# Kernel optimization log

Measured on AMD Instinct MI355X. Metric: run time of the kernel, lower is better.

The kernel has to match this reference:

```python
import jax, jax.numpy as jnp
import numpy as np


def _seg_mean(h_src, src, dst, n_dst):
    # gather neighbor features along edges, then segment-mean onto dst nodes
    msgs = h_src[src]                                  # [E, F]
    s = jax.ops.segment_sum(msgs, dst, num_segments=n_dst)
    deg = jax.ops.segment_sum(jnp.ones_like(dst, dtype=h_src.dtype), dst, num_segments=n_dst)
    return s / jnp.maximum(deg, 1.0)[:, None]          # zero-degree -> 0


def _sage_conv(h_src, h_dst, src, dst, n_dst, W, b):
    h_N = _seg_mean(h_src, src, dst, n_dst)            # [n_dst, F]
    h_total = jnp.concatenate([h_dst, h_N], axis=1)    # [n_dst, 2F]
    return h_total @ W + b


def setup_inputs() -> dict:
    key = jax.random.key(0)
    ks = jax.random.split(key, 10)
    n_src1, n_dst1, n_dst2 = 200000, 50000, 10000
    E1, E2 = 1000000, 200000
    in_f, h_f, n_cls = 256, 256, 64
    x = jax.random.normal(ks[0], (n_src1, in_f), dtype=jnp.float32)
    W1 = jax.random.normal(ks[1], (2 * in_f, h_f), dtype=jnp.float32) * (1.0 / np.sqrt(2 * in_f))
    b1 = jax.random.normal(ks[2], (h_f,), dtype=jnp.float32) * 0.01
    W2 = jax.random.normal(ks[3], (2 * h_f, n_cls), dtype=jnp.float32) * (1.0 / np.sqrt(2 * h_f))
    b2 = jax.random.normal(ks[4], (n_cls,), dtype=jnp.float32) * 0.01
    src1 = jax.random.randint(ks[5], (E1,), 0, n_src1, dtype=jnp.int32)
    dst1 = jax.random.randint(ks[6], (E1,), 0, n_dst1, dtype=jnp.int32)
    src2 = jax.random.randint(ks[7], (E2,), 0, n_dst1, dtype=jnp.int32)
    dst2 = jax.random.randint(ks[8], (E2,), 0, n_dst2, dtype=jnp.int32)
    return {"x": x, "W1": W1, "b1": b1, "W2": W2, "b2": b2,
            "src1": src1, "dst1": dst1, "src2": src2, "dst2": dst2,
            "n_dst1": n_dst1, "n_dst2": n_dst2}


def reference(x, W1, b1, W2, b2, src1, dst1, src2, dst2, n_dst1, n_dst2):
    h_dst = x[:n_dst1]
    h = _sage_conv(x, h_dst, src1, dst1, n_dst1, W1, b1)
    h = jax.nn.relu(h)
    h_dst2 = h[:n_dst2]
    out = _sage_conv(h, h_dst2, src2, dst2, n_dst2, W2, b2)
    return out
```

## Files before the change

### kernel.cpp

```cpp
#include <hip/hip_runtime.h>
#include <hip/hip_bf16.h>

#define N_DST1 50000
#define N_DST2 10000
#define FEAT   256

typedef unsigned int u32;
typedef __attribute__((ext_vector_type(4))) float f32x4;
typedef __attribute__((ext_vector_type(8))) short bf16x8;

__device__ __forceinline__ ushort f2bf(float f) {
    u32 u = __float_as_uint(f);
    u32 r = (u + 0x7FFFu + ((u >> 16) & 1u)) >> 16;
    return (ushort)r;
}
__device__ __forceinline__ float bf2f(ushort u) {
    return __uint_as_float(((u32)u) << 16);
}

__device__ __forceinline__ void gload_lds16(const void* g, void* l) {
    __builtin_amdgcn_global_load_lds(
        (const __attribute__((address_space(1))) u32*)g,
        (__attribute__((address_space(3))) u32*)l, 16, 0, 0);
}

__global__ __launch_bounds__(256) void prep_kernel(
    const float* __restrict__ x, ushort* __restrict__ xb, u32* __restrict__ xq,
    int n8, int n8h,
    const int* __restrict__ dst1, int E1, int* __restrict__ deg1,
    const int* __restrict__ dst2, int E2, int* __restrict__ deg2)
{
    int gid = blockIdx.x * blockDim.x + threadIdx.x;
    if (gid < n8) {
        const f32x4* p = (const f32x4*)x + (size_t)gid * 2;
        f32x4 a = __builtin_nontemporal_load(p);
        f32x4 b = __builtin_nontemporal_load(p + 1);
        if (xq) {
            u32 w0 = 0, w1 = 0;
            w0 = __builtin_amdgcn_cvt_pk_fp8_f32(a.x, a.y, w0, false);
            w0 = __builtin_amdgcn_cvt_pk_fp8_f32(a.z, a.w, w0, true);
            w1 = __builtin_amdgcn_cvt_pk_fp8_f32(b.x, b.y, w1, false);
            w1 = __builtin_amdgcn_cvt_pk_fp8_f32(b.z, b.w, w1, true);
            uint2 wv; wv.x = w0; wv.y = w1;
            *((uint2*)xq + gid) = wv;
        }
        if (gid < n8h) {
            ushort4 lo = make_ushort4(f2bf(a.x), f2bf(a.y), f2bf(a.z), f2bf(a.w));
            ushort4 hi = make_ushort4(f2bf(b.x), f2bf(b.y), f2bf(b.z), f2bf(b.w));
            ushort4* q = (ushort4*)xb + (size_t)gid * 2;
            q[0] = lo; q[1] = hi;
        }
    } else {
        int e = gid - n8;
        if (e < E1) atomicAdd(&deg1[dst1[e]], 1);
        else {
            int k = e - E1;
            if (k < E2) atomicAdd(&deg2[dst2[k]], 1);
        }
    }
}

__global__ __launch_bounds__(1024) void scan_wt_kernel(
    const int* __restrict__ degA, int nA, int* __restrict__ offA, int* __restrict__ posA,
    const int* __restrict__ degB, int nB, int* __restrict__ offB, int* __restrict__ posB,
    const float* __restrict__ W1, ushort* __restrict__ W1T,
    const float* __restrict__ W2, ushort* __restrict__ W2T)
{
    if (blockIdx.x >= 2) {
        int k = blockIdx.x - 2;
        int t = threadIdx.x;
        if (t < 256) W1T[(size_t)t * 512 + k] = f2bf(W1[(size_t)k * 256 + t]);
        else if (t < 320) {
            int n = t - 256;
            W2T[(size_t)n * 512 + k] = f2bf(W2[(size_t)k * 64 + n]);
        }
        return;
    }
    const int* deg = (blockIdx.x == 0) ? degA : degB;
    int*       off = (blockIdx.x == 0) ? offA : offB;
    int*       pos = (blockIdx.x == 0) ? posA : posB;
    int n = (blockIdx.x == 0) ? nA : nB;
    int n4 = n >> 2;

    __shared__ int wsum[16];
    __shared__ int carry_s;
    int t = threadIdx.x;
    int lane = t & 63, wid = t >> 6;
    if (t == 0) carry_s = 0;
    __syncthreads();
    for (int base = 0; base < n4; base += 1024) {
        int i = base + t;
        int4 v = make_int4(0, 0, 0, 0);
        if (i < n4) v = reinterpret_cast<const int4*>(deg)[i];
        int tot = v.x + v.y + v.z + v.w;
        int s = tot;
        #pragma unroll
        for (int d = 1; d < 64; d <<= 1) {
            int u = __shfl_up(s, d, 64);
            if (lane >= d) s += u;
        }
        if (lane == 63) wsum[wid] = s;
        __syncthreads();
        if (wid == 0 && lane < 16) {
            int ws = wsum[lane];
            #pragma unroll
            for (int d = 1; d < 16; d <<= 1) {
                int u = __shfl_up(ws, d, 64);
                if (lane >= d) ws += u;
            }
            wsum[lane] = ws;
        }
        __syncthreads();
        int waveoff = (wid == 0) ? 0 : wsum[wid - 1];
        int carry = carry_s;
        int base0 = carry + waveoff + s - tot;
        if (i < n4) {
            int4 e;
            e.x = base0;
            e.y = base0 + v.x;
            e.z = base0 + v.x + v.y;
            e.w = base0 + v.x + v.y + v.z;
            reinterpret_cast<int4*>(off)[i] = e;
            reinterpret_cast<int4*>(pos)[i] = e;
        }
        __syncthreads();
        if (t == 0) carry_s = carry + wsum[15];
        __syncthreads();
    }
    if (t == 0) off[n] = carry_s;
}

__global__ void scatter_csr2_kernel(const int* __restrict__ src1, const int* __restrict__ dst1,
                                    int E1, int* __restrict__ pos1, int* __restrict__ csr1,
                                    const int* __restrict__ src2, const int* __restrict__ dst2,
                                    int E2, int* __restrict__ pos2, int* __restrict__ csr2) {
    int i = blockIdx.x * blockDim.x + threadIdx.x;
    if (i < E1) {
        int slot = atomicAdd(&pos1[dst1[i]], 1);
        csr1[slot] = src1[i];
    } else {
        int k = i - E1;
        if (k < E2) {
            int slot = atomicAdd(&pos2[dst2[k]], 1);
            csr2[slot] = src2[k];
        }
    }
}

__global__ __launch_bounds__(512) void seg_mean_fp8_kernel(
    const u32* __restrict__ Xq, const int* __restrict__ off,
    const int* __restrict__ csr, ushort* __restrict__ out, int ndst)
{
    int wid = threadIdx.x >> 6;
    int d = blockIdx.x * 8 + wid;
    if (d >= ndst) return;
    int l = threadIdx.x & 63;
    int sub = l >> 4;
    int lg = l & 15;
    int beg = off[d], end = off[d + 1];
    float acc[16];
    #pragma unroll
    for (int q = 0; q < 16; ++q) acc[q] = 0.f;
    for (int j = beg; j < end; j += 4) {
        int idx = j + sub;
        int r = csr[min(idx, end - 1)];
        uint4 v = *reinterpret_cast<const uint4*>(Xq + (size_t)r * 64 + lg * 4);
        float m = (idx < end) ? 1.f : 0.f;
        u32 wv[4] = {v.x, v.y, v.z, v.w};
        #pragma unroll
        for (int w = 0; w < 4; ++w) {
            auto p01 = __builtin_amdgcn_cvt_pk_f32_fp8(wv[w], false);
            auto p23 = __builtin_amdgcn_cvt_pk_f32_fp8(wv[w], true);
            acc[w * 4 + 0] += m * p01[0];
            acc[w * 4 + 1] += m * p01[1];
            acc[w * 4 + 2] += m * p23[0];
            acc[w * 4 + 3] += m * p23[1];
        }
    }
    #pragma unroll
    for (int q = 0; q < 16; ++q) {
        acc[q] += __shfl_xor(acc[q], 16);
        acc[q] += __shfl_xor(acc[q], 32);
    }
    if (l < 16) {
        float sc = 1.0f / (float)max(end - beg, 1);
        bf16x8 o0, o1;
        #pragma unroll
        for (int q = 0; q < 8; ++q) {
            o0[q] = (short)f2bf(acc[q] * sc);
            o1[q] = (short)f2bf(acc[8 + q] * sc);
        }
        ushort* base = out + (size_t)d * FEAT + lg * 16;
        *reinterpret_cast<bf16x8*>(base) = o0;
        *reinterpret_cast<bf16x8*>(base + 8) = o1;
    }
}

__global__ __launch_bounds__(512) void seg_mean_bf16_kernel(
    const ushort* __restrict__ X, const int* __restrict__ off,
    const int* __restrict__ csr, ushort* __restrict__ out, int ndst)
{
    int wid = threadIdx.x >> 6;
    int d = blockIdx.x * 8 + wid;
    if (d >= ndst) return;
    int l = threadIdx.x & 63;
    int half = l >> 5;
    int f8 = (l & 31) * 8;
    int beg = off[d], end = off[d + 1];
    float acc[8] = {0.f, 0.f, 0.f, 0.f, 0.f, 0.f, 0.f, 0.f};
    for (int j = beg; j < end; j += 8) {
        #pragma unroll
        for (int p = 0; p < 4; ++p) {
            int idx = j + p * 2 + half;
            int r = csr[min(idx, end - 1)];
            bf16x8 v = *reinterpret_cast<const bf16x8*>(&X[(size_t)r * FEAT + f8]);
            float m = (idx < end) ? 1.f : 0.f;
            #pragma unroll
            for (int q = 0; q < 8; ++q) acc[q] += m * bf2f((ushort)v[q]);
        }
    }
    #pragma unroll
    for (int q = 0; q < 8; ++q) acc[q] += __shfl_xor(acc[q], 32);
    if (l < 32) {
        float sc = 1.0f / (float)max(end - beg, 1);
        bf16x8 ov;
        #pragma unroll
        for (int q = 0; q < 8; ++q) ov[q] = (short)f2bf(acc[q] * sc);
        *reinterpret_cast<bf16x8*>(&out[(size_t)d * FEAT + f8]) = ov;
    }
}

__global__ void seg_mean_f32_kernel(const float* __restrict__ X, const int* __restrict__ off,
                                    const int* __restrict__ csr, ushort* __restrict__ out) {
    int d = blockIdx.x;
    int t = threadIdx.x;
    int beg = off[d], end = off[d + 1];
    float a0 = 0.f, a1 = 0.f, a2 = 0.f, a3 = 0.f;
    for (int j = beg; j < end; ++j) {
        int s = csr[j];
        float4 v = *reinterpret_cast<const float4*>(&X[(size_t)s * FEAT + t * 4]);
        a0 += v.x; a1 += v.y; a2 += v.z; a3 += v.w;
    }
    float sc = 1.0f / (float)max(end - beg, 1);
    ushort4 o = make_ushort4(f2bf(a0 * sc), f2bf(a1 * sc), f2bf(a2 * sc), f2bf(a3 * sc));
    *reinterpret_cast<ushort4*>(&out[(size_t)d * FEAT + t * 4]) = o;
}

template<int BM, int BN, int WGM, int WGN, bool RELU, bool OBF16>
__global__ __launch_bounds__(WGM * WGN * 64)
void gemm_mfma_kernel(const ushort* __restrict__ A0, const ushort* __restrict__ A1,
                      const ushort* __restrict__ BT, const float* __restrict__ bias,
                      ushort* __restrict__ Cb, float* __restrict__ Cf,
                      int M, int Nfull) {
    constexpr int NWAVE = WGM * WGN;
    constexpr int WM = BM / WGM;
    constexpr int WN = BN / WGN;
    constexpr int MF = WM / 16;
    constexpr int NF = WN / 16;
    constexpr int ACH = BM / 16;
    constexpr int BCH = BN / 16;

    __shared__ ushort Al[2][BM][32];
    __shared__ ushort Bl[2][BN][32];

    const int t = threadIdx.x;
    const int lane = t & 63;
    const int wid = t >> 6;
    const int wm = wid / WGN, wn = wid % WGN;
    const int lr = lane & 15, grp = lane >> 4;
    const int rowBase = blockIdx.y * BM;
    const int colBase = blockIdx.x * BN;

    f32x4 acc[MF][NF];
    #pragma unroll
    for (int m = 0; m < MF; ++m)
        #pragma unroll
        for (int n = 0; n < NF; ++n)
            acc[m][n] = (f32x4){0.f, 0.f, 0.f, 0.f};

    auto stage = [&](int buf, int kt) {
        const ushort* Asrc = (kt < 8) ? A0 : A1;
        const int kcol = (kt * 32) & 255;
        #pragma unroll
        for (int ch = wid; ch < ACH; ch += NWAVE) {
            int r = ch * 16 + (lane >> 2);
            int rg = min(rowBase + r, M - 1);
            int c = lane & 3;
            int ksw = (c ^ (r & 3)) * 8;
            gload_lds16(&Asrc[(size_t)rg * 256 + kcol + ksw], &Al[buf][ch * 16][0]);
        }
        #pragma unroll
        for (int ch = wid; ch < BCH; ch += NWAVE) {
            int r = ch * 16 + (lane >> 2);
            int c = lane & 3;
            int ksw = (c ^ (r & 3)) * 8;
            gload_lds16(&BT[(size_t)(colBase + r) * 512 + kt * 32 + ksw], &Bl[buf][ch * 16][0]);
        }
    };

    stage(0, 0);
    __syncthreads();

    int buf = 0;
    for (int kt = 0; kt < 16; ++kt) {
        if (kt + 1 < 16) stage(buf ^ 1, kt + 1);
        bf16x8 af[MF], bfr[NF];
        #pragma unroll
        for (int m = 0; m < MF; ++m) {
            int r = wm * WM + m * 16 + lr;
            af[m] = *reinterpret_cast<const bf16x8*>(
                (const char*)&Al[buf][0][0] + r * 64 + ((grp ^ (r & 3)) << 4));
        }
        #pragma unroll
        for (int n = 0; n < NF; ++n) {
            int r = wn * WN + n * 16 + lr;
            bfr[n] = *reinterpret_cast<const bf16x8*>(
                (const char*)&Bl[buf][0][0] + r * 64 + ((grp ^ (r & 3)) << 4));
        }
        #pragma unroll
        for (int m = 0; m < MF; ++m)
            #pragma unroll
            for (int n = 0; n < NF; ++n)
                acc[m][n] = __builtin_amdgcn_mfma_f32_16x16x32_bf16(af[m], bfr[n], acc[m][n], 0, 0, 0);
        __syncthreads();
        buf ^= 1;
    }

    #pragma unroll
    for (int m = 0; m < MF; ++m) {
        #pragma unroll
        for (int q = 0; q < 4; ++q) {
            int rowg = rowBase + wm * WM + m * 16 + grp * 4 + q;
            if (rowg >= M) continue;
            #pragma unroll
            for (int n = 0; n < NF; ++n) {
                int colg = colBase + wn * WN + n * 16 + lr;
                float v = acc[m][n][q] + bias[colg];
                if (RELU) v = fmaxf(v, 0.f);
                if (OBF16) Cb[(size_t)rowg * Nfull + colg] = f2bf(v);
                else       Cf[(size_t)rowg * Nfull + colg] = v;
            }
        }
    }
}

extern "C" void kernel_launch(void* const* d_in, const int* in_sizes, int n_in,
                              void* d_out, int out_size, void* d_ws, size_t ws_size,
                              hipStream_t stream) {
    const float* x  = (const float*)d_in[0];
    const float* W1 = (const float*)d_in[1];
    const float* b1 = (const float*)d_in[2];
    const float* W2 = (const float*)d_in[3];
    const float* b2 = (const float*)d_in[4];
    const int* src1 = (const int*)d_in[5];
    const int* dst1 = (const int*)d_in[6];
    const int* src2 = (const int*)d_in[7];
    const int* dst2 = (const int*)d_in[8];
    const int E1 = in_sizes[5];
    const int E2 = in_sizes[7];
    const int N_SRC1 = in_sizes[0] / FEAT;
    float* out = (float*)d_out;

    char* ws = (char*)d_ws;
    size_t o = 0;
    auto carve = [&](size_t bytes) { char* p = ws + o; o = (o + bytes + 255) & ~(size_t)255; return p; };
    int*    degs = (int*)   carve((size_t)(N_DST1 + N_DST2) * 4);
    int*    deg1 = degs;
    int*    deg2 = degs + N_DST1;
    int*    off1 = (int*)   carve((size_t)(N_DST1 + 1) * 4);
    int*    pos1 = (int*)   carve((size_t)N_DST1 * 4);
    int*    csr1 = (int*)   carve((size_t)E1 * 4);
    ushort* hN1b = (ushort*)carve((size_t)N_DST1 * FEAT * 2);
    ushort* hb   = (ushort*)carve((size_t)N_DST1 * FEAT * 2);
    int*    off2 = (int*)   carve((size_t)(N_DST2 + 1) * 4);
    int*    pos2 = (int*)   carve((size_t)N_DST2 * 4);
    int*    csr2 = (int*)   carve((size_t)E2 * 4);
    ushort* hN2b = (ushort*)carve((size_t)N_DST2 * FEAT * 2);
    ushort* W1T  = (ushort*)carve((size_t)256 * 512 * 2);
    ushort* W2T  = (ushort*)carve((size_t)64 * 512 * 2);
    ushort* xb = (ushort*)carve((size_t)N_DST1 * FEAT * 2);
    size_t q_bytes = (size_t)N_SRC1 * FEAT;
    bool fp8path = (o + q_bytes) <= ws_size;
    u32* xq = fp8path ? (u32*)carve(q_bytes) : nullptr;

    (void)hipMemsetAsync(degs, 0, (size_t)(N_DST1 + N_DST2) * 4, stream);
    {
        int n8  = (fp8path ? N_SRC1 : N_DST1) * FEAT / 8;
        int n8h = N_DST1 * FEAT / 8;
        int tot = n8 + E1 + E2;
        prep_kernel<<<(tot + 255) / 256, 256, 0, stream>>>(
            x, xb, xq, n8, n8h, dst1, E1, deg1, dst2, E2, deg2);
    }
    scan_wt_kernel<<<514, 1024, 0, stream>>>(deg1, N_DST1, off1, pos1,
                                             deg2, N_DST2, off2, pos2,
                                             W1, W1T, W2, W2T);
    scatter_csr2_kernel<<<(E1 + E2 + 255) / 256, 256, 0, stream>>>(
        src1, dst1, E1, pos1, csr1, src2, dst2, E2, pos2, csr2);

    if (fp8path)
        seg_mean_fp8_kernel<<<(N_DST1 + 7) / 8, 512, 0, stream>>>(xq, off1, csr1, hN1b, N_DST1);
    else
        seg_mean_f32_kernel<<<N_DST1, 64, 0, stream>>>(x, off1, csr1, hN1b);
    gemm_mfma_kernel<128, 128, 2, 2, true, true><<<dim3(2, (N_DST1 + 127) / 128), 256, 0, stream>>>(
        xb, hN1b, W1T, b1, hb, nullptr, N_DST1, 256);

    seg_mean_bf16_kernel<<<(N_DST2 + 7) / 8, 512, 0, stream>>>(hb, off2, csr2, hN2b, N_DST2);
    gemm_mfma_kernel<64, 64, 2, 2, false, false><<<dim3(1, (N_DST2 + 63) / 64), 256, 0, stream>>>(
        hb, hN2b, W2T, b2, nullptr, out, N_DST2, 64);
}
```

Baseline: 310.7 us.

## Vectorize edge loops by four, unroll fp8 gather by two, widen GEMM1 tile

The degree-count and CSR scatter kernels now have each thread load int4 vectors of dst/src and issue four atomics, so fewer threads launch and index loads are wider. The fp8 segment-mean loop handles two neighbor rows per sub-lane per iteration to keep more gathers in flight. The first GEMM moves to a 128x256 tile with 512 threads, so one block covers the whole output width and A is loaded once. The wider GEMM tile lowers the block count to about 391 and may raise register pressure. The unrolled gather uses more registers.

```diff
diff --git a/kernel.cpp b/kernel.cpp
--- a/kernel.cpp
+++ b/kernel.cpp
@@ -50,14 +50,29 @@
             ushort4* q = (ushort4*)xb + (size_t)gid * 2;
             q[0] = lo; q[1] = hi;
         }
-    } else {
-        int e = gid - n8;
-        if (e < E1) atomicAdd(&deg1[dst1[e]], 1);
-        else {
-            int k = e - E1;
-            if (k < E2) atomicAdd(&deg2[dst2[k]], 1);
-        }
-    }
+        return;
+    }
+    int e = gid - n8;
+    int e14 = E1 >> 2, e24 = E2 >> 2;
+    if (e < e14) {
+        int4 d4 = reinterpret_cast<const int4*>(dst1)[e];
+        atomicAdd(&deg1[d4.x], 1); atomicAdd(&deg1[d4.y], 1);
+        atomicAdd(&deg1[d4.z], 1); atomicAdd(&deg1[d4.w], 1);
+        return;
+    }
+    e -= e14;
+    if (e < e24) {
+        int4 d4 = reinterpret_cast<const int4*>(dst2)[e];
+        atomicAdd(&deg2[d4.x], 1); atomicAdd(&deg2[d4.y], 1);
+        atomicAdd(&deg2[d4.z], 1); atomicAdd(&deg2[d4.w], 1);
+        return;
+    }
+    e -= e24;
+    int r1 = E1 & 3;
+    if (e < r1) { atomicAdd(&deg1[dst1[E1 - r1 + e]], 1); return; }
+    e -= r1;
+    int r2 = E2 & 3;
+    if (e < r2) { atomicAdd(&deg2[dst2[E2 - r2 + e]], 1); return; }
 }
 
 __global__ __launch_bounds__(1024) void scan_wt_kernel(
@@ -134,16 +149,40 @@
                                     int E1, int* __restrict__ pos1, int* __restrict__ csr1,
                                     const int* __restrict__ src2, const int* __restrict__ dst2,
                                     int E2, int* __restrict__ pos2, int* __restrict__ csr2) {
-    int i = blockIdx.x * blockDim.x + threadIdx.x;
-    if (i < E1) {
-        int slot = atomicAdd(&pos1[dst1[i]], 1);
-        csr1[slot] = src1[i];
-    } else {
-        int k = i - E1;
-        if (k < E2) {
-            int slot = atomicAdd(&pos2[dst2[k]], 1);
-            csr2[slot] = src2[k];
-        }
+    int e = blockIdx.x * blockDim.x + threadIdx.x;
+    int e14 = E1 >> 2, e24 = E2 >> 2;
+    if (e < e14) {
+        int4 s4 = reinterpret_cast<const int4*>(src1)[e];
+        int4 d4 = reinterpret_cast<const int4*>(dst1)[e];
+        csr1[atomicAdd(&pos1[d4.x], 1)] = s4.x;
+        csr1[atomicAdd(&pos1[d4.y], 1)] = s4.y;
+        csr1[atomicAdd(&pos1[d4.z], 1)] = s4.z;
+        csr1[atomicAdd(&pos1[d4.w], 1)] = s4.w;
+        return;
+    }
+    e -= e14;
+    if (e < e24) {
+        int4 s4 = reinterpret_cast<const int4*>(src2)[e];
+        int4 d4 = reinterpret_cast<const int4*>(dst2)[e];
+        csr2[atomicAdd(&pos2[d4.x], 1)] = s4.x;
+        csr2[atomicAdd(&pos2[d4.y], 1)] = s4.y;
+        csr2[atomicAdd(&pos2[d4.z], 1)] = s4.z;
+        csr2[atomicAdd(&pos2[d4.w], 1)] = s4.w;
+        return;
+    }
+    e -= e24;
+    int r1 = E1 & 3;
+    if (e < r1) {
+        int i = E1 - r1 + e;
+        csr1[atomicAdd(&pos1[dst1[i]], 1)] = src1[i];
+        return;
+    }
+    e -= r1;
+    int r2 = E2 & 3;
+    if (e < r2) {
+        int i = E2 - r2 + e;
+        csr2[atomicAdd(&pos2[dst2[i]], 1)] = src2[i];
+        return;
     }
 }
 
@@ -161,20 +200,26 @@
     float acc[16];
     #pragma unroll
     for (int q = 0; q < 16; ++q) acc[q] = 0.f;
-    for (int j = beg; j < end; j += 4) {
-        int idx = j + sub;
-        int r = csr[min(idx, end - 1)];
-        uint4 v = *reinterpret_cast<const uint4*>(Xq + (size_t)r * 64 + lg * 4);
-        float m = (idx < end) ? 1.f : 0.f;
-        u32 wv[4] = {v.x, v.y, v.z, v.w};
+    for (int j = beg; j < end; j += 8) {
+        int i0 = j + sub, i1 = j + 4 + sub;
+        int r0 = csr[min(i0, end - 1)];
+        int r1 = csr[min(i1, end - 1)];
+        uint4 v0 = *reinterpret_cast<const uint4*>(Xq + (size_t)r0 * 64 + lg * 4);
+        uint4 v1 = *reinterpret_cast<const uint4*>(Xq + (size_t)r1 * 64 + lg * 4);
+        float m0 = (i0 < end) ? 1.f : 0.f;
+        float m1 = (i1 < end) ? 1.f : 0.f;
+        u32 w0[4] = {v0.x, v0.y, v0.z, v0.w};
+        u32 w1[4] = {v1.x, v1.y, v1.z, v1.w};
         #pragma unroll
         for (int w = 0; w < 4; ++w) {
-            auto p01 = __builtin_amdgcn_cvt_pk_f32_fp8(wv[w], false);
-            auto p23 = __builtin_amdgcn_cvt_pk_f32_fp8(wv[w], true);
-            acc[w * 4 + 0] += m * p01[0];
-            acc[w * 4 + 1] += m * p01[1];
-            acc[w * 4 + 2] += m * p23[0];
-            acc[w * 4 + 3] += m * p23[1];
+            auto a01 = __builtin_amdgcn_cvt_pk_f32_fp8(w0[w], false);
+            auto a23 = __builtin_amdgcn_cvt_pk_f32_fp8(w0[w], true);
+            auto b01 = __builtin_amdgcn_cvt_pk_f32_fp8(w1[w], false);
+            auto b23 = __builtin_amdgcn_cvt_pk_f32_fp8(w1[w], true);
+            acc[w * 4 + 0] += m0 * a01[0] + m1 * b01[0];
+            acc[w * 4 + 1] += m0 * a01[1] + m1 * b01[1];
+            acc[w * 4 + 2] += m0 * a23[0] + m1 * b23[0];
+            acc[w * 4 + 3] += m0 * a23[1] + m1 * b23[1];
         }
     }
     #pragma unroll
@@ -387,21 +432,24 @@
     {
         int n8  = (fp8path ? N_SRC1 : N_DST1) * FEAT / 8;
         int n8h = N_DST1 * FEAT / 8;
-        int tot = n8 + E1 + E2;
+        int tot = n8 + (E1 >> 2) + (E2 >> 2) + (E1 & 3) + (E2 & 3);
         prep_kernel<<<(tot + 255) / 256, 256, 0, stream>>>(
             x, xb, xq, n8, n8h, dst1, E1, deg1, dst2, E2, deg2);
     }
     scan_wt_kernel<<<514, 1024, 0, stream>>>(deg1, N_DST1, off1, pos1,
                                              deg2, N_DST2, off2, pos2,
                                              W1, W1T, W2, W2T);
-    scatter_csr2_kernel<<<(E1 + E2 + 255) / 256, 256, 0, stream>>>(
-        src1, dst1, E1, pos1, csr1, src2, dst2, E2, pos2, csr2);
+    {
+        int tot = (E1 >> 2) + (E2 >> 2) + (E1 & 3) + (E2 & 3);
+        scatter_csr2_kernel<<<(tot + 255) / 256, 256, 0, stream>>>(
+            src1, dst1, E1, pos1, csr1, src2, dst2, E2, pos2, csr2);
+    }
 
     if (fp8path)
         seg_mean_fp8_kernel<<<(N_DST1 + 7) / 8, 512, 0, stream>>>(xq, off1, csr1, hN1b, N_DST1);
     else
         seg_mean_f32_kernel<<<N_DST1, 64, 0, stream>>>(x, off1, csr1, hN1b);
-    gemm_mfma_kernel<128, 128, 2, 2, true, true><<<dim3(2, (N_DST1 + 127) / 128), 256, 0, stream>>>(
+    gemm_mfma_kernel<128, 256, 2, 4, true, true><<<dim3(1, (N_DST1 + 127) / 128), 512, 0, stream>>>(
         xb, hN1b, W1T, b1, hb, nullptr, N_DST1, 256);
 
     seg_mean_bf16_kernel<<<(N_DST2 + 7) / 8, 512, 0, stream>>>(hb, off2, csr2, hN2b, N_DST2);
```

After: 303.2 us. -2.4%, faster.
